# Kernel tuning notes

Hardware: AMD Instinct MI355X
Metric: run time of the kernel (lower is better)

The kernel has to match this reference:

```python
import jax, jax.numpy as jnp
import numpy as np

H = 16          # num_heads
BASE = 10000.0  # lrpe base
EPS = 1e-6      # rmsnorm eps


def setup_inputs() -> dict:
    key = jax.random.key(0)
    ks = jax.random.split(key, 8)
    b, n, d = 2, 2048, 1024
    hd = d // H
    s = 1.0 / np.sqrt(d)
    x = jax.random.normal(ks[0], (b, n, d), jnp.float32)
    wq = jax.random.normal(ks[1], (d, d), jnp.float32) * s
    wk = jax.random.normal(ks[2], (d, d), jnp.float32) * s
    wv = jax.random.normal(ks[3], (d, d), jnp.float32) * s
    wo = jax.random.normal(ks[4], (d, d), jnp.float32) * s
    wg1 = jax.random.normal(ks[5], (d, hd), jnp.float32) * s
    wg2 = jax.random.normal(ks[6], (hd, d), jnp.float32) * (1.0 / np.sqrt(hd))
    norm_w = jnp.ones((d,), jnp.float32)
    return {"x": x, "wq": wq, "wk": wk, "wv": wv, "wo": wo,
            "wg1": wg1, "wg2": wg2, "norm_w": norm_w}


def reference(x, wq, wk, wv, wo, wg1, wg2, norm_w):
    b, n, d = x.shape
    hd = d // H
    # projections + activations
    q = jax.nn.silu(x @ wq).reshape(b, n, H, hd)
    k = (x @ wk).reshape(b, n, H, hd)
    v = (x @ wv).reshape(b, n, H, hd)
    # vector decay via logcumsumexp over time (lse_state starts at 0 -> z[:,0]=0)
    f = jnp.concatenate([jnp.zeros((b, 1, H, hd), x.dtype), k], axis=1)  # (b,n+1,h,d)
    z = jax.lax.cumlogsumexp(f, axis=1)
    log_f = z[:, :-1] - z[:, 1:]          # (b,n,h,d), <= 0
    k = jnp.exp(k - z[:, 1:])             # normalized exp kernel keys
    # LRPE type 1 (cosine): d -> 2d, per-head theta slice
    theta = BASE ** (-2.0 / (H * hd) * jnp.arange(H * hd, dtype=x.dtype))
    theta = theta.reshape(H, hd)
    ang = jnp.arange(n, dtype=x.dtype)[:, None, None] * theta[None]  # (n,h,d)
    c, s_ = jnp.cos(ang), jnp.sin(ang)
    q = jnp.concatenate([q * c, q * s_], axis=-1)   # (b,n,h,2d)
    k = jnp.concatenate([k * c, k * s_], axis=-1)
    ld = jnp.concatenate([log_f, log_f], axis=-1)   # repeat '... d -> ... (g d)', g=2
    # lightning linear attention with vector decay: S_t = diag(exp(ld_t)) S_{t-1} + k_t v_t^T
    def step(S, inp):
        qt, kt, vt, lt = inp
        S = jnp.exp(lt)[..., None] * S + kt[..., None] * vt[..., None, :]
        o = jnp.einsum('bhe,bhev->bhv', qt, S)
        return S, o
    S0 = jnp.zeros((b, H, 2 * hd, hd), x.dtype)
    seq = (jnp.moveaxis(q, 1, 0), jnp.moveaxis(k, 1, 0),
           jnp.moveaxis(v, 1, 0), jnp.moveaxis(ld, 1, 0))
    _, o = jax.lax.scan(step, S0, seq)
    o = jnp.moveaxis(o, 0, 1).reshape(b, n, d)
    # fused gated group-RMSNorm (gate_pos='pre', sigmoid gate, num_groups=H)
    gate = (x @ wg1) @ wg2
    g = o * jax.nn.sigmoid(gate)
    gg = g.reshape(b, n, H, hd)
    rms = jnp.sqrt(jnp.mean(gg * gg, axis=-1, keepdims=True) + EPS)
    normed = (gg / rms).reshape(b, n, d) * norm_w
    return normed @ wo
```

## Files before the change

### kernel.cpp

```cpp
#include <hip/hip_runtime.h>
#include <math.h>

#define NH 16
#define HD 64
#define DMODEL 1024
#define NSEQ 2048
#define BATCH 2
#define CHUNK 32
#define NCH (NSEQ / CHUNK)
#define LN_BASE 9.210340371976184f

typedef __attribute__((ext_vector_type(8))) short bf16x8;
typedef __attribute__((ext_vector_type(8))) unsigned short u16x8;
typedef __attribute__((ext_vector_type(4))) float f32x4;

__device__ __forceinline__ unsigned short f2bf(float f) {
  union { float f; unsigned int u; } v; v.f = f;
  unsigned int u = v.u;
  unsigned int r = u + 0x7FFFu + ((u >> 16) & 1u);
  return (unsigned short)(r >> 16);
}
__device__ __forceinline__ float bf2f(unsigned short u) {
  union { unsigned int u; float f; } v; v.u = ((unsigned int)u) << 16;
  return v.f;
}

__device__ __forceinline__ void fast_sincos(float ang, float* s, float* c) {
  const float INV2PI = 0.15915494309189535f;
  const float TWOPI  = 6.283185307179586f;
  float rev = ang * INV2PI;
  rev = rev - floorf(rev);
  float ar = rev * TWOPI;
  *s = __sinf(ar);
  *c = __cosf(ar);
}

__device__ __forceinline__ void gload_lds16(const unsigned short* g,
                                            unsigned short* l) {
  __builtin_amdgcn_global_load_lds(
      (const __attribute__((address_space(1))) void*)g,
      (__attribute__((address_space(3))) void*)l, 16, 0, 0);
}

__global__ __launch_bounds__(256) void transpose_cvt5x(
    const float* __restrict__ s0, const float* __restrict__ s1,
    const float* __restrict__ s2, const float* __restrict__ s3,
    const float* __restrict__ xs,
    unsigned short* __restrict__ d0, unsigned short* __restrict__ d1,
    unsigned short* __restrict__ d2, unsigned short* __restrict__ d3,
    unsigned short* __restrict__ xd) {
  const int z = blockIdx.z;
  if (z == 4) {
    const int lin = blockIdx.y * 32 + blockIdx.x;
    const size_t base = (size_t)lin * 4096 + threadIdx.x * 4;
#pragma unroll
    for (int r = 0; r < 4; ++r) {
      float4 v = *(const float4*)(xs + base + r * 1024);
      unsigned short* o = xd + base + r * 1024;
      o[0] = f2bf(v.x); o[1] = f2bf(v.y); o[2] = f2bf(v.z); o[3] = f2bf(v.w);
    }
    return;
  }
  const float* in = (z == 0) ? s0 : (z == 1) ? s1 : (z == 2) ? s2 : s3;
  unsigned short* out = (z == 0) ? d0 : (z == 1) ? d1 : (z == 2) ? d2 : d3;
  __shared__ float tl[32][33];
  const int t = threadIdx.x;
  const int ci = t & 31, ri = t >> 5;
  const int br = blockIdx.y * 32, bc = blockIdx.x * 32;
#pragma unroll
  for (int rr = 0; rr < 4; ++rr)
    tl[ri + rr * 8][ci] = in[(size_t)(br + ri + rr * 8) * DMODEL + bc + ci];
  __syncthreads();
#pragma unroll
  for (int rr = 0; rr < 4; ++rr) {
    const int orow = bc + ri + rr * 8;
    const int ocol = br + ci;
    out[(size_t)orow * DMODEL + ocol] = f2bf(tl[ci][ri + rr * 8]);
  }
}

__global__ __launch_bounds__(256) void wg_gemmT(const float* __restrict__ A,
                                                const float* __restrict__ B,
                                                unsigned short* __restrict__ Ct) {
  __shared__ float As[64][65];
  __shared__ float Bs[64][64];
  const int tid = threadIdx.x;
  const int tx = tid & 15, ty = tid >> 4;
  const int bm = (blockIdx.x >> 4) * 64;
  const int bn = (blockIdx.x & 15) * 64;

  {
    const int row = tid >> 2;
    const int ko = (tid & 3) * 16;
    const float* src = A + (size_t)(bm + row) * 64 + ko;
#pragma unroll
    for (int q = 0; q < 4; ++q) {
      float4 v = *(const float4*)(src + q * 4);
      As[row][ko + q * 4 + 0] = v.x; As[row][ko + q * 4 + 1] = v.y;
      As[row][ko + q * 4 + 2] = v.z; As[row][ko + q * 4 + 3] = v.w;
    }
  }
  {
    const int k = tid >> 2;
    const int co = (tid & 3) * 16;
    const float* src = B + (size_t)k * DMODEL + bn + co;
#pragma unroll
    for (int q = 0; q < 4; ++q)
      *(float4*)&Bs[k][co + q * 4] = *(const float4*)(src + q * 4);
  }
  __syncthreads();

  float acc[4][4];
#pragma unroll
  for (int i = 0; i < 4; ++i)
#pragma unroll
    for (int j = 0; j < 4; ++j) acc[i][j] = 0.f;
#pragma unroll 8
  for (int kk = 0; kk < 64; ++kk) {
    float a[4], b[4];
#pragma unroll
    for (int i = 0; i < 4; ++i) a[i] = As[ty * 4 + i][kk];
#pragma unroll
    for (int j = 0; j < 4; ++j) b[j] = Bs[kk][tx * 4 + j];
#pragma unroll
    for (int i = 0; i < 4; ++i)
#pragma unroll
      for (int j = 0; j < 4; ++j) acc[i][j] = fmaf(a[i], b[j], acc[i][j]);
  }
#pragma unroll
  for (int j = 0; j < 4; ++j) {
    unsigned long long pk =
        (unsigned long long)f2bf(acc[0][j])
      | ((unsigned long long)f2bf(acc[1][j]) << 16)
      | ((unsigned long long)f2bf(acc[2][j]) << 32)
      | ((unsigned long long)f2bf(acc[3][j]) << 48);
    *(unsigned long long*)&Ct[(size_t)(bn + tx * 4 + j) * DMODEL + bm + ty * 4] = pk;
  }
}

__global__ __launch_bounds__(256, 4) void gemm_bf16_fused(
    const unsigned short* __restrict__ A, const unsigned short* __restrict__ Bt,
    unsigned short* __restrict__ B0, unsigned short* __restrict__ B1,
    unsigned short* __restrict__ B2, unsigned short* __restrict__ B3,
    int M, int Ntot, int K) {
  __shared__ unsigned short As[128][64];
  __shared__ unsigned short Bs[128][64];
  const int tid = threadIdx.x;
  const int l = tid & 63;
  const int w = tid >> 6;
  const int wr = (w >> 1) * 64;
  const int wc = (w & 1) * 64;

  const int orig = blockIdx.x;
  const int xcd = orig & 7;
  const int idx = orig >> 3;
  const int bm = ((xcd >> 1) * 8 + (idx & 7)) * 128;
  const int bn = ((xcd & 1) * 16 + (idx >> 3)) * 128;

  const int lrow = l >> 3;
  const int cd = l & 7;
  const int cl = cd ^ lrow;

  f32x4 acc[4][4];
#pragma unroll
  for (int m = 0; m < 4; ++m)
#pragma unroll
    for (int n = 0; n < 4; ++n) acc[m][n] = (f32x4){0.f, 0.f, 0.f, 0.f};

  for (int k0 = 0; k0 < K; k0 += 64) {
    __syncthreads();
#pragma unroll
    for (int c = 0; c < 4; ++c) {
      const int row = w * 32 + c * 8 + lrow;
      unsigned short* la = (unsigned short*)As + (w * 32 + c * 8) * 64 + l * 8;
      gload_lds16(A + (size_t)(bm + row) * K + k0 + cl * 8, la);
    }
#pragma unroll
    for (int c = 0; c < 4; ++c) {
      const int row = w * 32 + c * 8 + lrow;
      unsigned short* lb = (unsigned short*)Bs + (w * 32 + c * 8) * 64 + l * 8;
      gload_lds16(Bt + (size_t)(bn + row) * K + k0 + cl * 8, lb);
    }
    __syncthreads();

#pragma unroll
    for (int ks = 0; ks < 2; ++ks) {
      bf16x8 af[4], bfr[4];
#pragma unroll
      for (int m = 0; m < 4; ++m) {
        const int r = wr + m * 16 + (l & 15);
        const int phys = (ks * 4 + (l >> 4)) ^ (r & 7);
        af[m] = *(const bf16x8*)&As[r][phys * 8];
      }
#pragma unroll
      for (int n = 0; n < 4; ++n) {
        const int r = wc + n * 16 + (l & 15);
        const int phys = (ks * 4 + (l >> 4)) ^ (r & 7);
        bfr[n] = *(const bf16x8*)&Bs[r][phys * 8];
      }
#pragma unroll
      for (int m = 0; m < 4; ++m)
#pragma unroll
        for (int n = 0; n < 4; ++n)
          acc[m][n] = __builtin_amdgcn_mfma_f32_16x16x32_bf16(af[m], bfr[n], acc[m][n], 0, 0, 0);
    }
  }

#pragma unroll
  for (int m = 0; m < 4; ++m) {
    const int row0 = bm + wr + m * 16 + (l >> 4) * 4;
#pragma unroll
    for (int n = 0; n < 4; ++n) {
      const int colw = wc + n * 16 + (l & 15);
#pragma unroll
      for (int r = 0; r < 4; ++r) {
        float x = acc[m][n][r];
        const int nb = bn >> 10;
        unsigned short* Bb = (nb == 0) ? B0 : (nb == 1) ? B1 : (nb == 2) ? B2 : B3;
        const int col = (bn & 1023) + colw;
        if (nb == 0) x = x / (1.f + expf(-x));
        Bb[(size_t)(row0 + r) * DMODEL + col] = f2bf(x);
      }
    }
  }
}

__global__ __launch_bounds__(256, 6) void gemm_bf16_wo(
    const unsigned short* __restrict__ A, const unsigned short* __restrict__ Bt,
    float* __restrict__ C, int M, int N, int K) {
  __shared__ unsigned short As[32][64];
  __shared__ unsigned short Bs[128][64];
  const int tid = threadIdx.x;
  const int l = tid & 63;
  const int w = tid >> 6;
  const int wr = (w >> 1) * 16;
  const int wc = (w & 1) * 64;

  const int nwg = gridDim.x;
  const int orig = blockIdx.x;
  const int swz = (orig & 7) * (nwg >> 3) + (orig >> 3);
  const int ntn = N >> 7;
  const int bm = (swz / ntn) * 32;
  const int bn = (swz % ntn) * 128;

  const int lrow = l >> 3;
  const int cd = l & 7;
  const int cl = cd ^ lrow;

  f32x4 acc[4];
#pragma unroll
  for (int n = 0; n < 4; ++n) acc[n] = (f32x4){0.f, 0.f, 0.f, 0.f};

  for (int k0 = 0; k0 < K; k0 += 64) {
    __syncthreads();
    {
      const int row = w * 8 + lrow;
      unsigned short* la = (unsigned short*)As + (w * 8) * 64 + l * 8;
      gload_lds16(A + (size_t)(bm + row) * K + k0 + cl * 8, la);
    }
#pragma unroll
    for (int c = 0; c < 4; ++c) {
      const int row = w * 32 + c * 8 + lrow;
      unsigned short* lb = (unsigned short*)Bs + (w * 32 + c * 8) * 64 + l * 8;
      gload_lds16(Bt + (size_t)(bn + row) * K + k0 + cl * 8, lb);
    }
    __syncthreads();

#pragma unroll
    for (int ks = 0; ks < 2; ++ks) {
      bf16x8 af, bfr[4];
      {
        const int r = wr + (l & 15);
        const int phys = (ks * 4 + (l >> 4)) ^ (r & 7);
        af = *(const bf16x8*)&As[r][phys * 8];
      }
#pragma unroll
      for (int n = 0; n < 4; ++n) {
        const int r = wc + n * 16 + (l & 15);
        const int phys = (ks * 4 + (l >> 4)) ^ (r & 7);
        bfr[n] = *(const bf16x8*)&Bs[r][phys * 8];
      }
#pragma unroll
      for (int n = 0; n < 4; ++n)
        acc[n] = __builtin_amdgcn_mfma_f32_16x16x32_bf16(af, bfr[n], acc[n], 0, 0, 0);
    }
  }

  {
    const int row0 = bm + wr + (l >> 4) * 4;
#pragma unroll
    for (int n = 0; n < 4; ++n) {
      const int col = bn + wc + n * 16 + (l & 15);
#pragma unroll
      for (int r = 0; r < 4; ++r)
        C[(size_t)(row0 + r) * N + col] = acc[n][r];
    }
  }
}

template <int ACT>
__global__ __launch_bounds__(256) void gemm_f32(const float* __restrict__ A,
                                                const float* __restrict__ B,
                                                float* __restrict__ C,
                                                int M, int N, int K) {
  __shared__ __align__(16) float As[16][128];
  __shared__ __align__(16) float Bs[16][128];
  const int tid = threadIdx.x;
  const int tx = tid & 15;
  const int ty = tid >> 4;
  const int bm = blockIdx.y * 128;
  const int bn = blockIdx.x * 128;

  float acc[8][8];
#pragma unroll
  for (int i = 0; i < 8; ++i)
#pragma unroll
    for (int j = 0; j < 8; ++j) acc[i][j] = 0.f;

  for (int k0 = 0; k0 < K; k0 += 16) {
    {
      const int row = tid >> 1;
      const int ko = (tid & 1) * 8;
      const float* src = A + (size_t)(bm + row) * K + k0 + ko;
      float4 a0 = *(const float4*)src;
      float4 a1 = *(const float4*)(src + 4);
      As[ko + 0][row] = a0.x; As[ko + 1][row] = a0.y;
      As[ko + 2][row] = a0.z; As[ko + 3][row] = a0.w;
      As[ko + 4][row] = a1.x; As[ko + 5][row] = a1.y;
      As[ko + 6][row] = a1.z; As[ko + 7][row] = a1.w;
    }
    {
      const int kr = tid >> 4;
      const int no = (tid & 15) * 8;
      float4 b0 = make_float4(0.f, 0.f, 0.f, 0.f);
      float4 b1 = b0;
      if (no < N) {
        const float* src = B + (size_t)(k0 + kr) * N + bn + no;
        b0 = *(const float4*)src;
        b1 = *(const float4*)(src + 4);
      }
      *(float4*)&Bs[kr][no] = b0;
      *(float4*)&Bs[kr][no + 4] = b1;
    }
    __syncthreads();
#pragma unroll
    for (int kk = 0; kk < 16; ++kk) {
      float a[8], b[8];
      *(float4*)&a[0] = *(const float4*)&As[kk][ty * 8];
      *(float4*)&a[4] = *(const float4*)&As[kk][ty * 8 + 4];
      *(float4*)&b[0] = *(const float4*)&Bs[kk][tx * 8];
      *(float4*)&b[4] = *(const float4*)&Bs[kk][tx * 8 + 4];
#pragma unroll
      for (int i = 0; i < 8; ++i)
#pragma unroll
        for (int j = 0; j < 8; ++j) acc[i][j] = fmaf(a[i], b[j], acc[i][j]);
    }
    __syncthreads();
  }

#pragma unroll
  for (int i = 0; i < 8; ++i) {
    const int row = bm + ty * 8 + i;
#pragma unroll
    for (int j = 0; j < 8; j += 4) {
      const int col = bn + tx * 8 + j;
      if (col < N) {
        float4 r;
        float* rv = (float*)&r;
#pragma unroll
        for (int q = 0; q < 4; ++q) {
          float x = acc[i][j + q];
          if (ACT == 1) x = x / (1.f + expf(-x));
          rv[q] = x;
        }
        *(float4*)&C[(size_t)row * N + col] = r;
      }
    }
  }
}

__global__ __launch_bounds__(256) void chunk_partial(
    const unsigned short* __restrict__ kb, float* __restrict__ partial) {
  const int blk = blockIdx.x;
  const int b = blk >> 8;
  const int rem = blk & 255;
  const int c = rem >> 2;
  const int seg = rem & 3;
  const int ch = seg * 256 + threadIdx.x;
  const unsigned short* base = kb + ((size_t)(b * NSEQ + c * CHUNK)) * DMODEL + ch;
  float acc = 0.f;
  for (int s = 0; s < CHUNK; ++s)
    acc += expf(bf2f(base[(size_t)s * DMODEL]));
  partial[((size_t)(b * NCH + c)) * DMODEL + ch] = acc;
}

__global__ __launch_bounds__(256) void chunk_zoff(const float* __restrict__ partial,
                                                  float* __restrict__ zoff) {
  const int g = blockIdx.x * 256 + threadIdx.x;
  const int b = g >> 10, dd = g & 1023;
  const size_t base = (size_t)b * NCH * DMODEL + dd;
  float vals[NCH];
#pragma unroll
  for (int c = 0; c < NCH; ++c)
    vals[c] = partial[base + (size_t)c * DMODEL];
  float run = 1.0f;
#pragma unroll
  for (int c = 0; c < NCH; ++c) {
    zoff[base + (size_t)c * DMODEL] = run;
    run += vals[c];
  }
}

__global__ __launch_bounds__(256) void chunk_attn(
    const unsigned short* __restrict__ qb, const unsigned short* __restrict__ kb,
    const unsigned short* __restrict__ vb, const float* __restrict__ zoff,
    unsigned short* __restrict__ qp, unsigned short* __restrict__ G,
    unsigned short* __restrict__ ob) {
  const int bidx = blockIdx.x;
  const int bh = bidx / NCH, c = bidx % NCH;
  const int b = bh >> 4, h = bh & 15;
  const int c0 = h * HD;

  __shared__ float sk[CHUNK][64];
  __shared__ float ps[4][64];
  __shared__ __align__(16) unsigned short qplds[CHUNK][136];
  __shared__ __align__(16) unsigned short khlds[CHUNK][136];
  __shared__ __align__(16) unsigned short kht[128][40];
  __shared__ __align__(16) unsigned short vt[64][40];
  __shared__ __align__(16) unsigned short slds[CHUNK][40];

  const int tid = threadIdx.x;
  const int l = tid & 63;
  const int w = tid >> 6;

  for (int idx = tid; idx < CHUNK * 64; idx += 256) {
    const int s = idx >> 6, dd2 = idx & 63;
    const size_t g = ((size_t)(b * NSEQ + c * CHUNK + s)) * DMODEL + c0 + dd2;
    sk[s][dd2] = bf2f(kb[g]);
    vt[dd2][s] = vb[g];
  }
  __syncthreads();

  const int dd = l;
  const int wq_ = w;
  {
    float a = 0.f;
#pragma unroll
    for (int i = 0; i < CHUNK / 4; ++i) a += expf(sk[wq_ * (CHUNK / 4) + i][dd]);
    ps[wq_][dd] = a;
  }
  __syncthreads();
  {
    float z = zoff[((size_t)(b * NCH + c)) * DMODEL + c0 + dd];
    for (int q2 = 0; q2 < wq_; ++q2) z += ps[q2][dd];
    const float theta = expf(-2.0f * (float)(c0 + dd) * (1.0f / 1024.0f) * LN_BASE);
#pragma unroll 2
    for (int i = 0; i < CHUNK / 4; ++i) {
      const int s = wq_ * (CHUNK / 4) + i;
      const int t = c * CHUNK + s;
      const float ek = expf(sk[s][dd]);
      z += ek;
      float sn, cs_;
      fast_sincos((float)t * theta, &sn, &cs_);
      const float qv = bf2f(qb[((size_t)(b * NSEQ + t)) * DMODEL + c0 + dd]);
      const float inv = 1.0f / z;
      const unsigned short kcb = f2bf(ek * cs_);
      const unsigned short ksb = f2bf(ek * sn);
      const unsigned short qcb = f2bf(qv * cs_ * inv);
      const unsigned short qsb = f2bf(qv * sn * inv);
      khlds[s][dd] = kcb;
      khlds[s][64 + dd] = ksb;
      kht[dd][s] = kcb;
      kht[64 + dd][s] = ksb;
      qplds[s][dd] = qcb;
      qplds[s][64 + dd] = qsb;
      unsigned short* qpo = qp + ((size_t)bidx * CHUNK + s) * 128;
      qpo[dd] = qcb;
      qpo[64 + dd] = qsb;
    }
  }
  __syncthreads();

  {
    const int mw = w >> 1, nw = w & 1;
    f32x4 sd = (f32x4){0.f, 0.f, 0.f, 0.f};
#pragma unroll
    for (int ks = 0; ks < 4; ++ks) {
      bf16x8 aq = *(const bf16x8*)&qplds[mw * 16 + (l & 15)][(l >> 4) * 8 + ks * 32];
      bf16x8 bk = *(const bf16x8*)&khlds[nw * 16 + (l & 15)][(l >> 4) * 8 + ks * 32];
      sd = __builtin_amdgcn_mfma_f32_16x16x32_bf16(aq, bk, sd, 0, 0, 0);
    }
    const int trow = mw * 16 + (l >> 4) * 4;
    const int scol = nw * 16 + (l & 15);
#pragma unroll
    for (int r = 0; r < 4; ++r) {
      const float v = (scol <= trow + r) ? sd[r] : 0.f;
      slds[trow + r][scol] = f2bf(v);
    }
  }

  {
    unsigned short* go = G + (size_t)bidx * 8192;
    const bf16x8 bv = *(const bf16x8*)&vt[w * 16 + (l & 15)][(l >> 4) * 8];
    const int jc = w * 16 + (l & 15);
#pragma unroll
    for (int et = 0; et < 8; ++et) {
      bf16x8 ak = *(const bf16x8*)&kht[et * 16 + (l & 15)][(l >> 4) * 8];
      f32x4 gd = (f32x4){0.f, 0.f, 0.f, 0.f};
      gd = __builtin_amdgcn_mfma_f32_16x16x32_bf16(ak, bv, gd, 0, 0, 0);
      const int e0r = et * 16 + (l >> 4) * 4;
      unsigned long long pk =
          (unsigned long long)f2bf(gd[0])
        | ((unsigned long long)f2bf(gd[1]) << 16)
        | ((unsigned long long)f2bf(gd[2]) << 32)
        | ((unsigned long long)f2bf(gd[3]) << 48);
      *(unsigned long long*)(go + (size_t)jc * 128 + e0r) = pk;
    }
  }
  __syncthreads();

  {
    const bf16x8 bv = *(const bf16x8*)&vt[w * 16 + (l & 15)][(l >> 4) * 8];
    const int jc = w * 16 + (l & 15);
#pragma unroll
    for (int tt = 0; tt < 2; ++tt) {
      bf16x8 as = *(const bf16x8*)&slds[tt * 16 + (l & 15)][(l >> 4) * 8];
      f32x4 od = (f32x4){0.f, 0.f, 0.f, 0.f};
      od = __builtin_amdgcn_mfma_f32_16x16x32_bf16(as, bv, od, 0, 0, 0);
      const int trow = tt * 16 + (l >> 4) * 4;
#pragma unroll
      for (int r = 0; r < 4; ++r)
        ob[((size_t)(b * NSEQ + c * CHUNK + trow + r)) * DMODEL + c0 + jc] = f2bf(od[r]);
    }
  }
}

__global__ __launch_bounds__(256) void chunk_prefix(unsigned short* __restrict__ G) {
  const int g = blockIdx.x * 256 + threadIdx.x;
  const int bh = g >> 12;
  const int e2 = (g & 4095) * 2;
  unsigned int* base = (unsigned int*)(G + (size_t)bh * NCH * 8192 + e2);
  unsigned int vals[NCH];
#pragma unroll
  for (int c = 0; c < NCH; ++c)
    vals[c] = base[(size_t)c * 4096];
  float run0 = 0.f, run1 = 0.f;
#pragma unroll
  for (int c = 0; c < NCH; ++c) {
    base[(size_t)c * 4096] =
        (unsigned int)f2bf(run0) | ((unsigned int)f2bf(run1) << 16);
    run0 += bf2f((unsigned short)(vals[c] & 0xFFFFu));
    run1 += bf2f((unsigned short)(vals[c] >> 16));
  }
}

__global__ __launch_bounds__(256) void chunk_inter_norm(
    const unsigned short* __restrict__ qp, const unsigned short* __restrict__ S0t,
    const unsigned short* __restrict__ ob, const unsigned short* __restrict__ gate,
    const float* __restrict__ norm_w, unsigned short* __restrict__ outb) {
  const int bidx = blockIdx.x;
  const int bh = bidx / NCH, c = bidx % NCH;
  const int b = bh >> 4, h = bh & 15;
  const int c0 = h * HD;

  const int tid = threadIdx.x;
  const int l = tid & 63;
  const int w = tid >> 6;
  const int mw = w >> 1;
  const int nw = w & 1;

  const unsigned short* qpb = qp + (size_t)bidx * CHUNK * 128;
  const unsigned short* s0b = S0t + (size_t)bidx * 8192;

  f32x4 acc[2];
  acc[0] = (f32x4){0.f, 0.f, 0.f, 0.f};
  acc[1] = (f32x4){0.f, 0.f, 0.f, 0.f};
#pragma unroll
  for (int ks = 0; ks < 4; ++ks) {
    const int ko = ks * 32 + (l >> 4) * 8;
    bf16x8 xa = *(const bf16x8*)(qpb + (size_t)(mw * 16 + (l & 15)) * 128 + ko);
#pragma unroll
    for (int n = 0; n < 2; ++n) {
      const int j = (nw * 2 + n) * 16 + (l & 15);
      bf16x8 yb = *(const bf16x8*)(s0b + (size_t)j * 128 + ko);
      acc[n] = __builtin_amdgcn_mfma_f32_16x16x32_bf16(xa, yb, acc[n], 0, 0, 0);
    }
  }

  __shared__ float ssh[2][32];
  float gval[2][4];
  float ssr[4];
#pragma unroll
  for (int r = 0; r < 4; ++r) {
    ssr[r] = 0.f;
    const int row = mw * 16 + (l >> 4) * 4 + r;
    const size_t rowg = ((size_t)(b * NSEQ + c * CHUNK + row)) * DMODEL + c0;
#pragma unroll
    for (int n = 0; n < 2; ++n) {
      const int col = (nw * 2 + n) * 16 + (l & 15);
      const float o = acc[n][r] + bf2f(ob[rowg + col]);
      const float gv = bf2f(gate[rowg + col]);
      const float g = o / (1.f + expf(-gv));
      gval[n][r] = g;
      ssr[r] = fmaf(g, g, ssr[r]);
    }
  }
#pragma unroll
  for (int r = 0; r < 4; ++r) {
    ssr[r] += __shfl_xor(ssr[r], 1);
    ssr[r] += __shfl_xor(ssr[r], 2);
    ssr[r] += __shfl_xor(ssr[r], 4);
    ssr[r] += __shfl_xor(ssr[r], 8);
  }
  if ((l & 15) == 0) {
#pragma unroll
    for (int r = 0; r < 4; ++r)
      ssh[nw][mw * 16 + (l >> 4) * 4 + r] = ssr[r];
  }
  __syncthreads();
#pragma unroll
  for (int r = 0; r < 4; ++r) {
    const int row = mw * 16 + (l >> 4) * 4 + r;
    const float ss = ssr[r] + ssh[nw ^ 1][row];
    const float inv = 1.0f / sqrtf(ss * (1.0f / 64.0f) + 1e-6f);
    const size_t rowg = ((size_t)(b * NSEQ + c * CHUNK + row)) * DMODEL + c0;
#pragma unroll
    for (int n = 0; n < 2; ++n) {
      const int col = (nw * 2 + n) * 16 + (l & 15);
      outb[rowg + col] = f2bf(gval[n][r] * inv * norm_w[c0 + col]);
    }
  }
}

__global__ __launch_bounds__(256) void scan_kernel(const float* __restrict__ qb,
                                                   const float* __restrict__ kb,
                                                   const float* __restrict__ vb,
                                                   float* __restrict__ ob) {
  const int bh = blockIdx.x;
  const int b = bh >> 4;
  const int h = bh & 15;
  const int c0 = h * HD;

  __shared__ float sk[64][64];
  __shared__ float sq[64][64];
  __shared__ float sv[64][64];
  __shared__ float kh[128];
  __shared__ float qph[128];
  __shared__ float vsh[64];
  __shared__ float opart[4][64];

  const int tid = threadIdx.x;
  const int lane = tid & 63;
  const int w = tid >> 6;
  const int e0 = w * 32;

  float T[32];
#pragma unroll
  for (int i = 0; i < 32; ++i) T[i] = 0.f;

  float zrun = 1.0f;
  float theta_v = 0.f;
  if (tid < 64) theta_v = expf(-2.0f * (float)(c0 + tid) * (1.0f / 1024.0f) * LN_BASE);

  for (int t0 = 0; t0 < NSEQ; t0 += 64) {
    __syncthreads();
    for (int idx = tid; idx < 64 * 64; idx += 256) {
      const int tl = idx >> 6;
      const int dd = idx & 63;
      const size_t g = ((size_t)(b * NSEQ + t0 + tl)) * DMODEL + c0 + dd;
      sk[tl][dd] = kb[g];
      sq[tl][dd] = qb[g];
      sv[tl][dd] = vb[g];
    }
    __syncthreads();

    for (int tl = 0; tl < 64; ++tl) {
      const int t = t0 + tl;
      if (tid < 64) {
        const int dd = tid;
        const float kr = sk[tl][dd];
        const float ek = expf(kr);
        zrun += ek;
        const float inv = 1.0f / zrun;
        float cs_, sn;
        fast_sincos((float)t * theta_v, &sn, &cs_);
        const float qv = sq[tl][dd];
        kh[dd] = ek * cs_;
        kh[64 + dd] = ek * sn;
        qph[dd] = qv * cs_ * inv;
        qph[64 + dd] = qv * sn * inv;
        vsh[dd] = sv[tl][dd];
      }
      __syncthreads();

      const float vj = vsh[lane];
      float accj = 0.f;
#pragma unroll
      for (int i = 0; i < 32; ++i) {
        T[i] = fmaf(kh[e0 + i], vj, T[i]);
        accj = fmaf(qph[e0 + i], T[i], accj);
      }
      opart[w][lane] = accj;
      __syncthreads();

      if (tid < 64) {
        const float o = opart[0][tid] + opart[1][tid] + opart[2][tid] + opart[3][tid];
        ob[((size_t)(b * NSEQ + t)) * DMODEL + c0 + tid] = o;
      }
    }
  }
}

__global__ __launch_bounds__(256) void gated_rmsnorm_f32(
    const float* __restrict__ o, const float* __restrict__ gate,
    const float* __restrict__ norm_w, float* __restrict__ outf) {
  const int gidx = blockIdx.x * 4 + (threadIdx.x >> 6);
  const int lane = threadIdx.x & 63;
  const size_t base = (size_t)gidx * 64 + lane;
  const float ov = o[base];
  const float gv = gate[base];
  const float g = ov / (1.f + expf(-gv));
  float ss = g * g;
#pragma unroll
  for (int off = 32; off; off >>= 1) ss += __shfl_xor(ss, off);
  const float rms = sqrtf(ss * (1.0f / 64.0f) + 1e-6f);
  const int cch = (gidx & 15) * 64 + lane;
  outf[base] = g / rms * norm_w[cch];
}

extern "C" void kernel_launch(void* const* d_in, const int* in_sizes, int n_in,
                              void* d_out, int out_size, void* d_ws, size_t ws_size,
                              hipStream_t stream) {
  const float* x      = (const float*)d_in[0];
  const float* wq     = (const float*)d_in[1];
  const float* wk     = (const float*)d_in[2];
  const float* wv     = (const float*)d_in[3];
  const float* wo     = (const float*)d_in[4];
  const float* wg1    = (const float*)d_in[5];
  const float* wg2    = (const float*)d_in[6];
  const float* norm_w = (const float*)d_in[7];
  float* out = (float*)d_out;

  const int M = BATCH * NSEQ;
  const size_t SZ = (size_t)M * DMODEL;
  const size_t WSZ = (size_t)DMODEL * DMODEL;

  float* qbuf = (float*)d_ws;
  float* kbuf = qbuf + SZ;
  float* vbuf = kbuf + SZ;
  float* obuf = vbuf + SZ;
  float* gbuf = obuf + SZ;
  float* g1   = gbuf + SZ;
  float* part = g1 + (size_t)M * HD;
  float* zoff = part + (size_t)BATCH * NCH * DMODEL;
  float* qpb  = zoff + (size_t)BATCH * NCH * DMODEL;
  float* Gb   = qpb + (size_t)BATCH * NH * NCH * CHUNK * 128;
  float* f32_end = Gb + (size_t)BATCH * NH * NCH * 8192;

  unsigned short* xbf   = (unsigned short*)f32_end;
  unsigned short* wAll  = xbf + SZ;
  unsigned short* wqT   = wAll;
  unsigned short* wkT   = wAll + WSZ;
  unsigned short* wvT   = wAll + 2 * WSZ;
  unsigned short* WgT   = wAll + 3 * WSZ;
  unsigned short* woT   = wAll + 4 * WSZ;
  unsigned short* nrmbf = woT + WSZ;
  unsigned short* u16_end = nrmbf + SZ;

  const size_t need_full = (size_t)((char*)u16_end - (char*)d_ws);

  unsigned short* qbuf16 = (unsigned short*)qbuf;
  unsigned short* kbuf16 = (unsigned short*)kbuf;
  unsigned short* vbuf16 = (unsigned short*)vbuf;
  unsigned short* obuf16 = (unsigned short*)obuf;
  unsigned short* gbuf16 = (unsigned short*)gbuf;
  unsigned short* qpb16  = (unsigned short*)qpb;
  unsigned short* Gb16   = (unsigned short*)Gb;

  dim3 blk(256);
  dim3 grid_d((DMODEL + 127) / 128, (M + 127) / 128);
  dim3 grid_g1(1, (M + 127) / 128);

  const bool full_ok = ws_size >= need_full;

  if (full_ok) {
    wg_gemmT<<<dim3(256), blk, 0, stream>>>(wg1, wg2, WgT);
    transpose_cvt5x<<<dim3(DMODEL / 32, DMODEL / 32, 5), blk, 0, stream>>>(
        wq, wk, wv, wo, x, wqT, wkT, wvT, woT, xbf);
    gemm_bf16_fused<<<dim3((M / 128) * (4 * DMODEL / 128)), blk, 0, stream>>>(
        xbf, wAll, qbuf16, kbuf16, vbuf16, gbuf16, M, 4 * DMODEL, DMODEL);

    chunk_partial<<<dim3(BATCH * NCH * 4), blk, 0, stream>>>(kbuf16, part);
    chunk_zoff<<<dim3(8), blk, 0, stream>>>(part, zoff);
    chunk_attn<<<dim3(BATCH * NH * NCH), blk, 0, stream>>>(qbuf16, kbuf16, vbuf16,
                                                           zoff, qpb16, Gb16, obuf16);
    chunk_prefix<<<dim3(BATCH * NH * 8192 / 512), blk, 0, stream>>>(Gb16);
    chunk_inter_norm<<<dim3(BATCH * NH * NCH), blk, 0, stream>>>(
        qpb16, Gb16, obuf16, gbuf16, norm_w, nrmbf);

    gemm_bf16_wo<<<dim3((M / 32) * (DMODEL / 128)), blk, 0, stream>>>(
        nrmbf, woT, out, M, DMODEL, DMODEL);
  } else {
    gemm_f32<1><<<grid_d, blk, 0, stream>>>(x, wq, qbuf, M, DMODEL, DMODEL);
    gemm_f32<0><<<grid_d, blk, 0, stream>>>(x, wk, kbuf, M, DMODEL, DMODEL);
    gemm_f32<0><<<grid_d, blk, 0, stream>>>(x, wv, vbuf, M, DMODEL, DMODEL);
    gemm_f32<0><<<grid_g1, blk, 0, stream>>>(x, wg1, g1, M, HD, DMODEL);
    gemm_f32<0><<<grid_d, blk, 0, stream>>>(g1, wg2, gbuf, M, DMODEL, HD);
    scan_kernel<<<dim3(BATCH * NH), blk, 0, stream>>>(qbuf, kbuf, vbuf, obuf);
    float* nrm = kbuf;
    gated_rmsnorm_f32<<<dim3(M * NH / 4), blk, 0, stream>>>(obuf, gbuf, norm_w, nrm);
    gemm_f32<0><<<grid_d, blk, 0, stream>>>(nrm, wo, out, M, DMODEL, DMODEL);
  }
}
```

Baseline: 135.5 us.

## Compute gate as low-rank two-step product instead of folding wg1@wg2 into fused GEMM

Rather than forming the full 1024x1024 product of wg1 and wg2 and running it as a fourth N-block of the fused projection GEMM, the gate is now computed as (x @ wg1) then @ wg2. Two small bf16 MFMA kernels handle this, and the transpose kernel gains two z-slices to convert wg1 and wg2. This drops the fp32 weight-product kernel and a quarter of the big GEMM's FLOPs, since the rank-64 path costs far less. In exchange there are extra launches and a g1 intermediate rounded to bf16, which adds a second rounding step to the gate.

```diff
diff --git a/kernel.cpp b/kernel.cpp
--- a/kernel.cpp
+++ b/kernel.cpp
@@ -42,13 +42,15 @@
       (__attribute__((address_space(3))) void*)l, 16, 0, 0);
 }
 
-__global__ __launch_bounds__(256) void transpose_cvt5x(
+__global__ __launch_bounds__(256) void transpose_cvt7(
     const float* __restrict__ s0, const float* __restrict__ s1,
     const float* __restrict__ s2, const float* __restrict__ s3,
-    const float* __restrict__ xs,
+    const float* __restrict__ xs, const float* __restrict__ wg1,
+    const float* __restrict__ wg2,
     unsigned short* __restrict__ d0, unsigned short* __restrict__ d1,
     unsigned short* __restrict__ d2, unsigned short* __restrict__ d3,
-    unsigned short* __restrict__ xd) {
+    unsigned short* __restrict__ xd, unsigned short* __restrict__ wg1T,
+    unsigned short* __restrict__ wg2T) {
   const int z = blockIdx.z;
   if (z == 4) {
     const int lin = blockIdx.y * 32 + blockIdx.x;
@@ -61,87 +63,173 @@
     }
     return;
   }
-  const float* in = (z == 0) ? s0 : (z == 1) ? s1 : (z == 2) ? s2 : s3;
-  unsigned short* out = (z == 0) ? d0 : (z == 1) ? d1 : (z == 2) ? d2 : d3;
+  const float* in;
+  unsigned short* out;
+  int R, Cn;
+  if (z < 4) {
+    in = (z == 0) ? s0 : (z == 1) ? s1 : (z == 2) ? s2 : s3;
+    out = (z == 0) ? d0 : (z == 1) ? d1 : (z == 2) ? d2 : d3;
+    R = DMODEL; Cn = DMODEL;
+  } else if (z == 5) {
+    if (blockIdx.x >= 2) return;
+    in = wg1; out = wg1T; R = DMODEL; Cn = 64;
+  } else {
+    if (blockIdx.y >= 2) return;
+    in = wg2; out = wg2T; R = 64; Cn = DMODEL;
+  }
   __shared__ float tl[32][33];
   const int t = threadIdx.x;
   const int ci = t & 31, ri = t >> 5;
   const int br = blockIdx.y * 32, bc = blockIdx.x * 32;
 #pragma unroll
   for (int rr = 0; rr < 4; ++rr)
-    tl[ri + rr * 8][ci] = in[(size_t)(br + ri + rr * 8) * DMODEL + bc + ci];
+    tl[ri + rr * 8][ci] = in[(size_t)(br + ri + rr * 8) * Cn + bc + ci];
   __syncthreads();
 #pragma unroll
   for (int rr = 0; rr < 4; ++rr) {
     const int orow = bc + ri + rr * 8;
     const int ocol = br + ci;
-    out[(size_t)orow * DMODEL + ocol] = f2bf(tl[ci][ri + rr * 8]);
-  }
-}
-
-__global__ __launch_bounds__(256) void wg_gemmT(const float* __restrict__ A,
-                                                const float* __restrict__ B,
-                                                unsigned short* __restrict__ Ct) {
-  __shared__ float As[64][65];
-  __shared__ float Bs[64][64];
+    out[(size_t)orow * R + ocol] = f2bf(tl[ci][ri + rr * 8]);
+  }
+}
+
+__global__ __launch_bounds__(256) void gemm_bf16_g1(
+    const unsigned short* __restrict__ A, const unsigned short* __restrict__ Bt,
+    unsigned short* __restrict__ C) {
+  __shared__ unsigned short As[16][64];
+  __shared__ unsigned short Bs[64][64];
   const int tid = threadIdx.x;
-  const int tx = tid & 15, ty = tid >> 4;
-  const int bm = (blockIdx.x >> 4) * 64;
-  const int bn = (blockIdx.x & 15) * 64;
+  const int l = tid & 63;
+  const int w = tid >> 6;
+  const int bm = blockIdx.x * 16;
+  const int K = DMODEL;
+
+  const int lrow = l >> 3;
+  const int cd = l & 7;
+  const int cl = cd ^ lrow;
+
+  f32x4 acc = (f32x4){0.f, 0.f, 0.f, 0.f};
+
+  for (int k0 = 0; k0 < K; k0 += 64) {
+    __syncthreads();
+    if (w < 2) {
+      const int row = w * 8 + lrow;
+      unsigned short* la = (unsigned short*)As + (w * 8) * 64 + l * 8;
+      gload_lds16(A + (size_t)(bm + row) * K + k0 + cl * 8, la);
+    }
+    {
+#pragma unroll
+      for (int c = 0; c < 2; ++c) {
+        const int row = w * 16 + c * 8 + lrow;
+        unsigned short* lb = (unsigned short*)Bs + (w * 16 + c * 8) * 64 + l * 8;
+        gload_lds16(Bt + (size_t)row * K + k0 + cl * 8, lb);
+      }
+    }
+    __syncthreads();
+
+#pragma unroll
+    for (int ks = 0; ks < 2; ++ks) {
+      bf16x8 af, bfr;
+      {
+        const int r = l & 15;
+        const int phys = (ks * 4 + (l >> 4)) ^ (r & 7);
+        af = *(const bf16x8*)&As[r][phys * 8];
+      }
+      {
+        const int r = w * 16 + (l & 15);
+        const int phys = (ks * 4 + (l >> 4)) ^ (r & 7);
+        bfr = *(const bf16x8*)&Bs[r][phys * 8];
+      }
+      acc = __builtin_amdgcn_mfma_f32_16x16x32_bf16(af, bfr, acc, 0, 0, 0);
+    }
+  }
 
   {
-    const int row = tid >> 2;
-    const int ko = (tid & 3) * 16;
-    const float* src = A + (size_t)(bm + row) * 64 + ko;
-#pragma unroll
-    for (int q = 0; q < 4; ++q) {
-      float4 v = *(const float4*)(src + q * 4);
-      As[row][ko + q * 4 + 0] = v.x; As[row][ko + q * 4 + 1] = v.y;
-      As[row][ko + q * 4 + 2] = v.z; As[row][ko + q * 4 + 3] = v.w;
-    }
-  }
+    const int row0 = bm + (l >> 4) * 4;
+    const int col = w * 16 + (l & 15);
+#pragma unroll
+    for (int r = 0; r < 4; ++r)
+      C[(size_t)(row0 + r) * 64 + col] = f2bf(acc[r]);
+  }
+}
+
+__global__ __launch_bounds__(256, 6) void gemm_bf16_gate(
+    const unsigned short* __restrict__ A, const unsigned short* __restrict__ Bt,
+    unsigned short* __restrict__ C, int M, int N, int K) {
+  __shared__ unsigned short As[32][64];
+  __shared__ unsigned short Bs[128][64];
+  const int tid = threadIdx.x;
+  const int l = tid & 63;
+  const int w = tid >> 6;
+  const int wr = (w >> 1) * 16;
+  const int wc = (w & 1) * 64;
+
+  const int nwg = gridDim.x;
+  const int orig = blockIdx.x;
+  const int swz = (orig & 7) * (nwg >> 3) + (orig >> 3);
+  const int ntn = N >> 7;
+  const int bm = (swz / ntn) * 32;
+  const int bn = (swz % ntn) * 128;
+
+  const int lrow = l >> 3;
+  const int cd = l & 7;
+  const int cl = cd ^ lrow;
+
+  f32x4 acc[4];
+#pragma unroll
+  for (int n = 0; n < 4; ++n) acc[n] = (f32x4){0.f, 0.f, 0.f, 0.f};
+
+  for (int k0 = 0; k0 < K; k0 += 64) {
+    __syncthreads();
+    {
+      const int row = w * 8 + lrow;
+      unsigned short* la = (unsigned short*)As + (w * 8) * 64 + l * 8;
+      gload_lds16(A + (size_t)(bm + row) * K + k0 + cl * 8, la);
+    }
+#pragma unroll
+    for (int c = 0; c < 4; ++c) {
+      const int row = w * 32 + c * 8 + lrow;
+      unsigned short* lb = (unsigned short*)Bs + (w * 32 + c * 8) * 64 + l * 8;
+      gload_lds16(Bt + (size_t)(bn + row) * K + k0 + cl * 8, lb);
+    }
+    __syncthreads();
+
+#pragma unroll
+    for (int ks = 0; ks < 2; ++ks) {
+      bf16x8 af, bfr[4];
+      {
+        const int r = wr + (l & 15);
+        const int phys = (ks * 4 + (l >> 4)) ^ (r & 7);
+        af = *(const bf16x8*)&As[r][phys * 8];
+      }
+#pragma unroll
+      for (int n = 0; n < 4; ++n) {
+        const int r = wc + n * 16 + (l & 15);
+        const int phys = (ks * 4 + (l >> 4)) ^ (r & 7);
+        bfr[n] = *(const bf16x8*)&Bs[r][phys * 8];
+      }
+#pragma unroll
+      for (int n = 0; n < 4; ++n)
+        acc[n] = __builtin_amdgcn_mfma_f32_16x16x32_bf16(af, bfr[n], acc[n], 0, 0, 0);
+    }
+  }
+
   {
-    const int k = tid >> 2;
-    const int co = (tid & 3) * 16;
-    const float* src = B + (size_t)k * DMODEL + bn + co;
-#pragma unroll
-    for (int q = 0; q < 4; ++q)
-      *(float4*)&Bs[k][co + q * 4] = *(const float4*)(src + q * 4);
-  }
-  __syncthreads();
-
-  float acc[4][4];
-#pragma unroll
-  for (int i = 0; i < 4; ++i)
-#pragma unroll
-    for (int j = 0; j < 4; ++j) acc[i][j] = 0.f;
-#pragma unroll 8
-  for (int kk = 0; kk < 64; ++kk) {
-    float a[4], b[4];
-#pragma unroll
-    for (int i = 0; i < 4; ++i) a[i] = As[ty * 4 + i][kk];
-#pragma unroll
-    for (int j = 0; j < 4; ++j) b[j] = Bs[kk][tx * 4 + j];
-#pragma unroll
-    for (int i = 0; i < 4; ++i)
-#pragma unroll
-      for (int j = 0; j < 4; ++j) acc[i][j] = fmaf(a[i], b[j], acc[i][j]);
-  }
-#pragma unroll
-  for (int j = 0; j < 4; ++j) {
-    unsigned long long pk =
-        (unsigned long long)f2bf(acc[0][j])
-      | ((unsigned long long)f2bf(acc[1][j]) << 16)
-      | ((unsigned long long)f2bf(acc[2][j]) << 32)
-      | ((unsigned long long)f2bf(acc[3][j]) << 48);
-    *(unsigned long long*)&Ct[(size_t)(bn + tx * 4 + j) * DMODEL + bm + ty * 4] = pk;
+    const int row0 = bm + wr + (l >> 4) * 4;
+#pragma unroll
+    for (int n = 0; n < 4; ++n) {
+      const int col = bn + wc + n * 16 + (l & 15);
+#pragma unroll
+      for (int r = 0; r < 4; ++r)
+        C[(size_t)(row0 + r) * N + col] = f2bf(acc[n][r]);
+    }
   }
 }
 
 __global__ __launch_bounds__(256, 4) void gemm_bf16_fused(
     const unsigned short* __restrict__ A, const unsigned short* __restrict__ Bt,
     unsigned short* __restrict__ B0, unsigned short* __restrict__ B1,
-    unsigned short* __restrict__ B2, unsigned short* __restrict__ B3,
+    unsigned short* __restrict__ B2,
     int M, int Ntot, int K) {
   __shared__ unsigned short As[128][64];
   __shared__ unsigned short Bs[128][64];
@@ -155,7 +243,7 @@
   const int xcd = orig & 7;
   const int idx = orig >> 3;
   const int bm = ((xcd >> 1) * 8 + (idx & 7)) * 128;
-  const int bn = ((xcd & 1) * 16 + (idx >> 3)) * 128;
+  const int bn = ((xcd & 1) * 12 + (idx >> 3)) * 128;
 
   const int lrow = l >> 3;
   const int cd = l & 7;
@@ -216,7 +304,7 @@
       for (int r = 0; r < 4; ++r) {
         float x = acc[m][n][r];
         const int nb = bn >> 10;
-        unsigned short* Bb = (nb == 0) ? B0 : (nb == 1) ? B1 : (nb == 2) ? B2 : B3;
+        unsigned short* Bb = (nb == 0) ? B0 : (nb == 1) ? B1 : B2;
         const int col = (bn & 1023) + colw;
         if (nb == 0) x = x / (1.f + expf(-x));
         Bb[(size_t)(row0 + r) * DMODEL + col] = f2bf(x);
@@ -762,7 +850,9 @@
   unsigned short* wqT   = wAll;
   unsigned short* wkT   = wAll + WSZ;
   unsigned short* wvT   = wAll + 2 * WSZ;
-  unsigned short* WgT   = wAll + 3 * WSZ;
+  unsigned short* wg1T  = wAll + 3 * WSZ;
+  unsigned short* wg2T  = wg1T + (size_t)64 * DMODEL;
+  unsigned short* g1b   = wg2T + (size_t)64 * DMODEL;
   unsigned short* woT   = wAll + 4 * WSZ;
   unsigned short* nrmbf = woT + WSZ;
   unsigned short* u16_end = nrmbf + SZ;
@@ -784,11 +874,13 @@
   const bool full_ok = ws_size >= need_full;
 
   if (full_ok) {
-    wg_gemmT<<<dim3(256), blk, 0, stream>>>(wg1, wg2, WgT);
-    transpose_cvt5x<<<dim3(DMODEL / 32, DMODEL / 32, 5), blk, 0, stream>>>(
-        wq, wk, wv, wo, x, wqT, wkT, wvT, woT, xbf);
-    gemm_bf16_fused<<<dim3((M / 128) * (4 * DMODEL / 128)), blk, 0, stream>>>(
-        xbf, wAll, qbuf16, kbuf16, vbuf16, gbuf16, M, 4 * DMODEL, DMODEL);
+    transpose_cvt7<<<dim3(32, 32, 7), blk, 0, stream>>>(
+        wq, wk, wv, wo, x, wg1, wg2, wqT, wkT, wvT, woT, xbf, wg1T, wg2T);
+    gemm_bf16_g1<<<dim3(M / 16), blk, 0, stream>>>(xbf, wg1T, g1b);
+    gemm_bf16_gate<<<dim3((M / 32) * (DMODEL / 128)), blk, 0, stream>>>(
+        g1b, wg2T, gbuf16, M, DMODEL, 64);
+    gemm_bf16_fused<<<dim3((M / 128) * (3 * DMODEL / 128)), blk, 0, stream>>>(
+        xbf, wAll, qbuf16, kbuf16, vbuf16, M, 3 * DMODEL, DMODEL);
 
     chunk_partial<<<dim3(BATCH * NCH * 4), blk, 0, stream>>>(kbuf16, part);
     chunk_zoff<<<dim3(8), blk, 0, stream>>>(part, zoff);
```

Result: no change. 135.8 us (+0.2%).
